# Performance work log

Hardware: AMD Instinct MI355X
Metric: run time of the kernel (lower is better)

## Reference

```python
import jax, jax.numpy as jnp
import numpy as np

B, GH, GW, DIM, NH = 1, 48, 64, 1536, 16
HD = DIM // NH          # 96
C = HD // 2             # 48, divisible by 3 as the rope split requires
L = max(GH, GW)


def setup_inputs() -> dict:
    key = jax.random.key(0)
    ks = jax.random.split(key, 6)
    x = jax.random.normal(ks[0], (B, GH * GW, DIM), jnp.float32)
    w_init = lambda k: jax.random.normal(k, (DIM, DIM), jnp.float32) * 0.02
    # rope frequency table: theta[p, j] = p / 10000^(j/C); freqs = exp(i*theta)
    pos = jnp.arange(L, dtype=jnp.float32)[:, None]
    inv = 10000.0 ** (-jnp.arange(C, dtype=jnp.float32) / C)
    theta = pos * inv[None, :]
    return {
        "x": x,
        "wq": w_init(ks[1]), "bq": jnp.zeros((DIM,), jnp.float32),
        "wk": w_init(ks[2]), "bk": jnp.zeros((DIM,), jnp.float32),
        "wv": w_init(ks[3]), "bv": jnp.zeros((DIM,), jnp.float32),
        "wo": w_init(ks[4]), "bo": jnp.zeros((DIM,), jnp.float32),
        "freqs_cos": jnp.cos(theta), "freqs_sin": jnp.sin(theta),
        "h": GH, "w": GW,
    }


def rope_apply_spatial(x, freqs_cos, freqs_sin, h, w):
    # x: [b, s, n, d] with s == h*w. Complex rotation done in real arithmetic.
    b, s, n, d = x.shape
    c = d // 2
    c3 = c // 3
    # channel groups: [0:c3] identity (ones), [c3:2c3] rotated by h-position,
    # [2c3:3c3] rotated by w-position  (matches freqs.split + cat in torch)
    cos_hw = jnp.concatenate([
        jnp.ones((h, w, c3), x.dtype),
        jnp.broadcast_to(freqs_cos[:h, None, c3:2 * c3], (h, w, c3)),
        jnp.broadcast_to(freqs_cos[None, :w, 2 * c3:3 * c3], (h, w, c3)),
    ], axis=-1).reshape(1, s, 1, c)
    sin_hw = jnp.concatenate([
        jnp.zeros((h, w, c3), x.dtype),
        jnp.broadcast_to(freqs_sin[:h, None, c3:2 * c3], (h, w, c3)),
        jnp.broadcast_to(freqs_sin[None, :w, 2 * c3:3 * c3], (h, w, c3)),
    ], axis=-1).reshape(1, s, 1, c)
    xc = x.reshape(b, s, n, c, 2)
    xr, xi = xc[..., 0], xc[..., 1]
    yr = xr * cos_hw - xi * sin_hw
    yi = xr * sin_hw + xi * cos_hw
    return jnp.stack([yr, yi], axis=-1).reshape(b, s, n, d)


def reference(x, wq, bq, wk, bk, wv, bv, wo, bo, freqs_cos, freqs_sin, h, w):
    b, s, _ = x.shape
    q = (x @ wq + bq).reshape(b, s, NH, HD)
    k = (x @ wk + bk).reshape(b, s, NH, HD)
    v = (x @ wv + bv).reshape(b, s, NH, HD)
    q = rope_apply_spatial(q, freqs_cos, freqs_sin, h, w)
    k = rope_apply_spatial(k, freqs_cos, freqs_sin, h, w)
    scale = 1.0 / jnp.sqrt(jnp.asarray(HD, q.dtype))
    scores = jnp.einsum('bqnd,bknd->bnqk', q, k) * scale  # [b, n, s, s]
    attn = jax.nn.softmax(scores, axis=-1)
    out = jnp.einsum('bnqk,bknd->bqnd', attn, v).reshape(b, s, NH * HD)
    return out @ wo + bo
```

## Files before the change

kernel.cpp:

```cpp
#include <hip/hip_runtime.h>
#include <math.h>

#define S_LEN 3072
#define DIM 1536
#define NHEADS 16
#define HDIM 96
#define NPAIR 48

typedef __attribute__((ext_vector_type(8))) _Float16 half8;
typedef __attribute__((ext_vector_type(4))) _Float16 half4v;
typedef __attribute__((ext_vector_type(2))) _Float16 half2v;
typedef __attribute__((ext_vector_type(4))) float f32x4;

__device__ inline void gload16(const void* g, void* l) {
    __builtin_amdgcn_global_load_lds(
        (const __attribute__((address_space(1))) void*)g,
        (__attribute__((address_space(3))) void*)l, 16, 0, 0);
}

__device__ inline uint4 gld128(const _Float16* p) {
    uint4 r;
    asm volatile("global_load_dwordx4 %0, %1, off"
                 : "=v"(r) : "v"(p));
    return r;
}

__global__ __launch_bounds__(256)
void convert_f32_f16(const float* __restrict__ src, _Float16* __restrict__ dst, int n4)
{
    int i = blockIdx.x * 256 + threadIdx.x;
    if (i < n4) {
        float4 v = *(const float4*)&src[(size_t)i * 4];
        half4v h = { (_Float16)v.x, (_Float16)v.y, (_Float16)v.z, (_Float16)v.w };
        *(half4v*)&dst[(size_t)i * 4] = h;
    }
}

__global__ __launch_bounds__(256)
void transpose_w(const float* __restrict__ w0, const float* __restrict__ w1,
                 const float* __restrict__ w2, const float* __restrict__ w3,
                 _Float16* __restrict__ wt)
{
    __shared__ _Float16 t[64][68];
    const int z = blockIdx.z;
    const float* W = (z == 0) ? w0 : (z == 1) ? w1 : (z == 2) ? w2 : w3;
    _Float16* O = wt + (size_t)z * DIM * DIM;
    const int k0 = blockIdx.y * 64, n0 = blockIdx.x * 64;
    const int tid = threadIdx.x;
    const int r = tid >> 4, c4 = (tid & 15) * 4;
#pragma unroll
    for (int g = 0; g < 4; g++) {
        int kk = r + g * 16;
        float4 v = *(const float4*)&W[(size_t)(k0 + kk) * DIM + n0 + c4];
        t[c4 + 0][kk] = (_Float16)v.x; t[c4 + 1][kk] = (_Float16)v.y;
        t[c4 + 2][kk] = (_Float16)v.z; t[c4 + 3][kk] = (_Float16)v.w;
    }
    __syncthreads();
    const int nr = tid >> 2, ks = (tid & 3) * 16;
#pragma unroll
    for (int s = 0; s < 4; s++)
        *(ushort4*)&O[(size_t)(n0 + nr) * DIM + k0 + ks + s * 4] =
            *(ushort4*)&t[nr][ks + s * 4];
}

template<bool QKV>
__global__ __launch_bounds__(512, 1)
void gemm256_f16(const _Float16* __restrict__ X,
                 const _Float16* __restrict__ W0t, const _Float16* __restrict__ W1t,
                 const _Float16* __restrict__ W2t,
                 const float* __restrict__ B0, const float* __restrict__ B1,
                 const float* __restrict__ B2,
                 const float* __restrict__ fc, const float* __restrict__ fs,
                 void* __restrict__ outv)
{
    __shared__ __align__(16) _Float16 AsB[2][256 * 64];
    __shared__ __align__(16) _Float16 BsB[2][256 * 64];

    const int tid = threadIdx.x;
    const int w = tid >> 6, lane = tid & 63;
    const int ln = lane & 15, quad = lane >> 4;
    const int bz = blockIdx.z;
    const _Float16* Wt = W0t; const float* bias = B0;
    if (QKV) { if (bz == 1) { Wt = W1t; bias = B1; } else if (bz == 2) { Wt = W2t; bias = B2; } }
    const int m0 = blockIdx.y * 256, n0 = blockIdx.x * 256;
    const int wm = w >> 2, wn = w & 3;
    const int row8 = lane >> 3, gch = (lane & 7) ^ row8;

    f32x4 acc[8][4];
#pragma unroll
    for (int i = 0; i < 8; i++)
#pragma unroll
        for (int j = 0; j < 4; j++) acc[i][j] = (f32x4){0.f, 0.f, 0.f, 0.f};

#pragma unroll
    for (int j = 0; j < 4; j++) {
        const int r = w * 32 + j * 8;
        gload16(X  + (size_t)(m0 + r + row8) * DIM + 0 + gch * 8, &AsB[0][r * 64]);
        gload16(Wt + (size_t)(n0 + r + row8) * DIM + 0 + gch * 8, &BsB[0][r * 64]);
    }
    asm volatile("s_waitcnt vmcnt(0)");
    __syncthreads();

    const int NKT = DIM / 64;
    for (int kt = 0; kt < NKT; ++kt) {
        const int cur = kt & 1;
        if (kt + 1 < NKT) {
            const int k0 = (kt + 1) * 64;
#pragma unroll
            for (int j = 0; j < 4; j++) {
                const int r = w * 32 + j * 8;
                gload16(X  + (size_t)(m0 + r + row8) * DIM + k0 + gch * 8, &AsB[cur ^ 1][r * 64]);
                gload16(Wt + (size_t)(n0 + r + row8) * DIM + k0 + gch * 8, &BsB[cur ^ 1][r * 64]);
            }
            __builtin_amdgcn_sched_barrier(0);
        }

#pragma unroll
        for (int ks = 0; ks < 2; ks++) {
            const int s8 = (((ks * 4 + quad) ^ (ln & 7))) * 8;
            half8 a[8], b[4];
#pragma unroll
            for (int mt = 0; mt < 8; mt++)
                a[mt] = *(const half8*)&AsB[cur][(wm * 128 + mt * 16 + ln) * 64 + s8];
#pragma unroll
            for (int nt = 0; nt < 4; nt++)
                b[nt] = *(const half8*)&BsB[cur][(wn * 64 + nt * 16 + ln) * 64 + s8];
#pragma unroll
            for (int mt = 0; mt < 8; mt++)
#pragma unroll
                for (int nt = 0; nt < 4; nt++)
                    acc[mt][nt] = __builtin_amdgcn_mfma_f32_16x16x32_f16(
                        a[mt], b[nt], acc[mt][nt], 0, 0, 0);
        }

        asm volatile("s_waitcnt vmcnt(0)");
        __syncthreads();
    }

#pragma unroll
    for (int nt = 0; nt < 4; nt++) {
        int col = n0 + wn * 64 + nt * 16 + ln;
        float bv = bias[col];
        int head = col / HDIM, hd = col % HDIM;
        int jc = hd >> 1;
        bool isreal = (ln & 1) == 0;
#pragma unroll
        for (int mt = 0; mt < 8; mt++) {
            int row0 = m0 + wm * 128 + mt * 16 + quad * 4;
            if (QKV && bz == 2) {
                half4v p;
#pragma unroll
                for (int r = 0; r < 4; r++) p[r] = (_Float16)(acc[mt][nt][r] + bv);
                *(half4v*)&((_Float16*)outv)[(((size_t)2 * NHEADS + head) * HDIM + hd) * S_LEN + row0] = p;
            } else if (QKV) {
                float v[4], vp[4];
#pragma unroll
                for (int r = 0; r < 4; r++) v[r] = acc[mt][nt][r] + bv;
#pragma unroll
                for (int r = 0; r < 4; r++) vp[r] = __shfl_xor(v[r], 1);
#pragma unroll
                for (int r = 0; r < 4; r++) {
                    int srow = row0 + r;
                    int pos = (jc < 32) ? (srow >> 6) : (srow & 63);
                    float c  = fc[pos * NPAIR + jc];
                    float sn = fs[pos * NPAIR + jc];
                    float xr = isreal ? v[r] : vp[r];
                    float xi = isreal ? vp[r] : v[r];
                    float rot = isreal ? (xr * c - xi * sn) : (xr * sn + xi * c);
                    float outval = (jc < 16) ? v[r] : rot;
                    ((_Float16*)outv)[(((size_t)bz * NHEADS + head) * S_LEN + srow) * HDIM + hd]
                        = (_Float16)outval;
                }
            } else {
#pragma unroll
                for (int r = 0; r < 4; r++)
                    ((float*)outv)[(size_t)(row0 + r) * DIM + col] = acc[mt][nt][r] + bv;
            }
        }
    }
}

__global__ __launch_bounds__(256, 2)
void attn_mfma_kernel(const _Float16* __restrict__ qh, const _Float16* __restrict__ kh,
                      const _Float16* __restrict__ vtg, _Float16* __restrict__ aoh)
{
    __shared__ __align__(16) _Float16 Kb[2][2][64 * 96];
    __shared__ __align__(16) _Float16 Vt[2][96][72];

    const int tid  = threadIdx.x;
    const int wid  = tid >> 6;
    const int p    = wid >> 1;
    const int wp   = wid & 1;
    const int lane = tid & 63;
    const int ln   = lane & 15;
    const int quad = lane >> 4;
    const int h    = blockIdx.y;
    const int q0   = blockIdx.x * 64;
    const float scale_ = 0.10206207261596577f * 1.4426950408889634f;
    const int NT = (S_LEN / 2) / 64;

    half8 aq[2][3];
#pragma unroll
    for (int qs = 0; qs < 2; qs++) {
        const _Float16* qrow = qh + (((size_t)h * S_LEN) + q0 + (wp * 2 + qs) * 16 + ln) * HDIM;
#pragma unroll
        for (int kb = 0; kb < 3; kb++) {
            half8 a = *(const half8*)&qrow[kb * 32 + quad * 8];
            half8 v;
#pragma unroll
            for (int i = 0; i < 8; i++) v[i] = (_Float16)((float)a[i] * scale_);
            aq[qs][kb] = v;
        }
    }

    f32x4 o[2][6];
#pragma unroll
    for (int qs = 0; qs < 2; qs++)
#pragma unroll
        for (int dn = 0; dn < 6; dn++) o[qs][dn] = (f32x4){0.f, 0.f, 0.f, 0.f};
    float m_[2] = {-INFINITY, -INFINITY}, l_[2] = {0.f, 0.f};

    const char* kbase = (const char*)(kh + ((size_t)h * S_LEN + p * (S_LEN / 2)) * HDIM);

    int koffb[6];
#pragma unroll
    for (int i = 0; i < 6; i++) {
        int pc = i * 128 + (tid & 127);
        int r  = pc / 12, c = pc - r * 12;
        int rm = r % 12;
        int cl = c - rm; if (cl < 0) cl += 12;
        koffb[i] = r * 192 + cl * 16;
    }
    const int A0 = (quad + ln) % 12;
    int ksel[3];
    ksel[0] = A0 * 16;
    { int t1 = A0 + 4; if (t1 >= 12) t1 -= 12; ksel[1] = t1 * 16; }
    { int t2 = A0 + 8; if (t2 >= 12) t2 -= 12; ksel[2] = t2 * 16; }

    const int tp = tid & 127;
    const int vd0 = tp >> 3, vc = tp & 7;
    const _Float16* vsrc0 = vtg + (size_t)h * HDIM * S_LEN + (size_t)vd0 * S_LEN
                          + p * (S_LEN / 2) + vc * 8;
    _Float16* vdst = &Vt[p][vd0][(vc ^ (vd0 & 7)) * 8];

#pragma unroll
    for (int i = 0; i < 6; i++)
        gload16(kbase + koffb[i], &Kb[p][0][i * 1024 + wp * 512]);
    uint4 vp0, vp1, vp2, vp3, vp4, vp5;
    vp0 = gld128(vsrc0 + 0 * 16 * S_LEN);
    vp1 = gld128(vsrc0 + 1 * 16 * S_LEN);
    vp2 = gld128(vsrc0 + 2 * 16 * S_LEN);
    vp3 = gld128(vsrc0 + 3 * 16 * S_LEN);
    vp4 = gld128(vsrc0 + 4 * 16 * S_LEN);
    vp5 = gld128(vsrc0 + 5 * 16 * S_LEN);
    asm volatile("s_waitcnt vmcnt(0)" ::: "memory");
    __builtin_amdgcn_sched_barrier(0);
    *(uint4*)(vdst + 0 * 16 * 72) = vp0;  *(uint4*)(vdst + 1 * 16 * 72) = vp1;
    *(uint4*)(vdst + 2 * 16 * 72) = vp2;  *(uint4*)(vdst + 3 * 16 * 72) = vp3;
    *(uint4*)(vdst + 4 * 16 * 72) = vp4;  *(uint4*)(vdst + 5 * 16 * 72) = vp5;
    __syncthreads();

    for (int kt = 0; kt < NT; ++kt) {
        const int cur = kt & 1;
        if (kt + 1 < NT) {
            const char* ks2 = kbase + (size_t)(kt + 1) * 12288;
#pragma unroll
            for (int i = 0; i < 6; i++)
                gload16(ks2 + koffb[i], &Kb[p][cur ^ 1][i * 1024 + wp * 512]);
            const _Float16* vs2 = vsrc0 + (kt + 1) * 64;
            vp0 = gld128(vs2 + 0 * 16 * S_LEN);
            vp1 = gld128(vs2 + 1 * 16 * S_LEN);
            vp2 = gld128(vs2 + 2 * 16 * S_LEN);
            vp3 = gld128(vs2 + 3 * 16 * S_LEN);
            vp4 = gld128(vs2 + 4 * 16 * S_LEN);
            vp5 = gld128(vs2 + 5 * 16 * S_LEN);
            __builtin_amdgcn_sched_barrier(0);
        }

        const char* Kc = (const char*)&Kb[p][cur][0];
        f32x4 s[2][4];
#pragma unroll
        for (int nb = 0; nb < 4; nb++) {
            const char* krow = Kc + (nb * 16 + ln) * 192;
            half8 ak0 = *(const half8*)(krow + ksel[(nb + 0) % 3]);
            half8 ak1 = *(const half8*)(krow + ksel[(nb + 1) % 3]);
            half8 ak2 = *(const half8*)(krow + ksel[(nb + 2) % 3]);
#pragma unroll
            for (int qs = 0; qs < 2; qs++) {
                f32x4 acc = (f32x4){0.f, 0.f, 0.f, 0.f};
                acc = __builtin_amdgcn_mfma_f32_16x16x32_f16(ak0, aq[qs][0], acc, 0, 0, 0);
                acc = __builtin_amdgcn_mfma_f32_16x16x32_f16(ak1, aq[qs][1], acc, 0, 0, 0);
                acc = __builtin_amdgcn_mfma_f32_16x16x32_f16(ak2, aq[qs][2], acc, 0, 0, 0);
                s[qs][nb] = acc;
            }
        }

        half4v ap[2][4];
#pragma unroll
        for (int qs = 0; qs < 2; qs++) {
            float ma = fmaxf(fmaxf(s[qs][0][0], s[qs][0][1]), fmaxf(s[qs][0][2], s[qs][0][3]));
            float mb = fmaxf(fmaxf(s[qs][1][0], s[qs][1][1]), fmaxf(s[qs][1][2], s[qs][1][3]));
            float mc = fmaxf(fmaxf(s[qs][2][0], s[qs][2][1]), fmaxf(s[qs][2][2], s[qs][2][3]));
            float md = fmaxf(fmaxf(s[qs][3][0], s[qs][3][1]), fmaxf(s[qs][3][2], s[qs][3][3]));
            float mx = fmaxf(fmaxf(ma, mb), fmaxf(mc, md));
            if (!__all(mx <= m_[qs] + 8.0f)) {
                mx = fmaxf(mx, __shfl_xor(mx, 16));
                mx = fmaxf(mx, __shfl_xor(mx, 32));
                float mn = fmaxf(m_[qs], mx);
                float al = __builtin_amdgcn_exp2f(m_[qs] - mn);
                m_[qs] = mn;
                l_[qs] *= al;
#pragma unroll
                for (int dn = 0; dn < 6; dn++)
#pragma unroll
                    for (int r = 0; r < 4; r++) o[qs][dn][r] *= al;
            }
            float rs = 0.f;
            float mq = m_[qs];
#pragma unroll
            for (int nb = 0; nb < 4; nb++) {
                float p0 = __builtin_amdgcn_exp2f(s[qs][nb][0] - mq);
                float p1 = __builtin_amdgcn_exp2f(s[qs][nb][1] - mq);
                float p2 = __builtin_amdgcn_exp2f(s[qs][nb][2] - mq);
                float p3 = __builtin_amdgcn_exp2f(s[qs][nb][3] - mq);
                rs += (p0 + p1) + (p2 + p3);
                half4v pk = { (_Float16)p0, (_Float16)p1, (_Float16)p2, (_Float16)p3 };
                ap[qs][nb] = pk;
            }
            l_[qs] += rs;
        }

#pragma unroll
        for (int nb = 0; nb < 4; nb++) {
            const int off = (((nb * 2 + (quad >> 1)) ^ (ln & 7)) * 8) + (quad & 1) * 4;
#pragma unroll
            for (int dn = 0; dn < 6; dn++) {
                half4v av = *(const half4v*)&Vt[p][dn * 16 + ln][off];
                o[0][dn] = __builtin_amdgcn_mfma_f32_16x16x16f16(av, ap[0][nb], o[0][dn], 0, 0, 0);
                o[1][dn] = __builtin_amdgcn_mfma_f32_16x16x16f16(av, ap[1][nb], o[1][dn], 0, 0, 0);
            }
        }

        __syncthreads();
        asm volatile("s_waitcnt vmcnt(0)" ::: "memory");
        __builtin_amdgcn_sched_barrier(0);
        if (kt + 1 < NT) {
            *(uint4*)(vdst + 0 * 16 * 72) = vp0;  *(uint4*)(vdst + 1 * 16 * 72) = vp1;
            *(uint4*)(vdst + 2 * 16 * 72) = vp2;  *(uint4*)(vdst + 3 * 16 * 72) = vp3;
            *(uint4*)(vdst + 4 * 16 * 72) = vp4;  *(uint4*)(vdst + 5 * 16 * 72) = vp5;
        }
        __syncthreads();
    }

    float lt[2];
#pragma unroll
    for (int qs = 0; qs < 2; qs++) {
        float l = l_[qs];
        l += __shfl_xor(l, 16);
        l += __shfl_xor(l, 32);
        lt[qs] = l;
    }
    float*  scr = (float*)&Kb[0][0][0];
    float2* mlb = (float2*)((char*)&Kb[0][0][0] + 26624);
    if (p == 1) {
#pragma unroll
        for (int qs = 0; qs < 2; qs++) {
            int row = (wp * 2 + qs) * 16 + ln;
            if (quad == 0) mlb[row] = make_float2(m_[qs], lt[qs]);
#pragma unroll
            for (int dn = 0; dn < 6; dn++)
                *(f32x4*)&scr[row * 100 + dn * 16 + quad * 4] = o[qs][dn];
        }
    }
    __syncthreads();
    if (p == 0) {
#pragma unroll
        for (int qs = 0; qs < 2; qs++) {
            int row = (wp * 2 + qs) * 16 + ln;
            float2 ml1 = mlb[row];
            float mm = fmaxf(m_[qs], ml1.x);
            float a0 = __builtin_amdgcn_exp2f(m_[qs] - mm);
            float a1 = __builtin_amdgcn_exp2f(ml1.x - mm);
            float li = 1.0f / (lt[qs] * a0 + ml1.y * a1);
            const size_t rowbase = (size_t)(q0 + row) * DIM + h * HDIM;
#pragma unroll
            for (int dn = 0; dn < 6; dn++) {
                f32x4 o1 = *(const f32x4*)&scr[row * 100 + dn * 16 + quad * 4];
                half4v pk;
#pragma unroll
                for (int r = 0; r < 4; r++)
                    pk[r] = (_Float16)((o[qs][dn][r] * a0 + o1[r] * a1) * li);
                *(half4v*)&aoh[rowbase + dn * 16 + quad * 4] = pk;
            }
        }
    }
}

extern "C" void kernel_launch(void* const* d_in, const int* in_sizes, int n_in,
                              void* d_out, int out_size, void* d_ws, size_t ws_size,
                              hipStream_t stream) {
    const float* x  = (const float*)d_in[0];
    const float* wq = (const float*)d_in[1];
    const float* bq = (const float*)d_in[2];
    const float* wk = (const float*)d_in[3];
    const float* bk = (const float*)d_in[4];
    const float* wv = (const float*)d_in[5];
    const float* bv = (const float*)d_in[6];
    const float* wo = (const float*)d_in[7];
    const float* bo = (const float*)d_in[8];
    const float* fc = (const float*)d_in[9];
    const float* fs = (const float*)d_in[10];
    float* out = (float*)d_out;

    const size_t per  = (size_t)NHEADS * S_LEN * HDIM;
    const size_t dim2 = (size_t)DIM * DIM;
    _Float16* hws  = (_Float16*)d_ws;
    _Float16* qkvh = hws;
    _Float16* qh   = qkvh;
    _Float16* kh   = qkvh + per;
    _Float16* vth  = qkvh + 2 * per;
    _Float16* xh   = hws + 3 * per;
    _Float16* wth  = hws + 4 * per;

    convert_f32_f16<<<(int)((S_LEN * DIM / 4 + 255) / 256), 256, 0, stream>>>(
        x, xh, S_LEN * DIM / 4);
    transpose_w<<<dim3(DIM / 64, DIM / 64, 4), 256, 0, stream>>>(wq, wk, wv, wo, wth);

    gemm256_f16<true><<<dim3(DIM / 256, S_LEN / 256, 3), 512, 0, stream>>>(
        xh, wth, wth + dim2, wth + 2 * dim2, bq, bk, bv, fc, fs, qkvh);
    attn_mfma_kernel<<<dim3(S_LEN / 64, NHEADS), 256, 0, stream>>>(qh, kh, vth, xh);
    gemm256_f16<false><<<dim3(DIM / 256, S_LEN / 256, 1), 512, 0, stream>>>(
        xh, wth + 3 * dim2, nullptr, nullptr, bo, nullptr, nullptr, fc, fs, out);
}
```

Measured before the change: 335.5 us.

## Deepen GEMM prefetch with partial vmcnt waits, XCD-aware block remap, smaller out-proj tile

Restructures the GEMM main loop so the load for tile kt+2 is issued right after the compute barrier, and waits use partial vmcnt counts instead of draining all outstanding loads. This keeps one tile's global-to-LDS transfer in flight during compute. The 1D grid is remapped so consecutive blocks on the same XCD get neighbouring tiles, improving L2 reuse. The output projection uses 128-row tiles, giving 144 workgroups instead of 72 to fill more CUs. The cost is a more fragile hand-tuned wait count and less per-block reuse in the output GEMM.

```diff
diff --git a/kernel.cpp b/kernel.cpp
--- a/kernel.cpp
+++ b/kernel.cpp
@@ -63,80 +63,96 @@
             *(ushort4*)&t[nr][ks + s * 4];
 }
 
-template<bool QKV>
+template<bool QKV, int BM>
 __global__ __launch_bounds__(512, 1)
-void gemm256_f16(const _Float16* __restrict__ X,
-                 const _Float16* __restrict__ W0t, const _Float16* __restrict__ W1t,
-                 const _Float16* __restrict__ W2t,
-                 const float* __restrict__ B0, const float* __restrict__ B1,
-                 const float* __restrict__ B2,
-                 const float* __restrict__ fc, const float* __restrict__ fs,
-                 void* __restrict__ outv)
+void gemm_pipe_f16(const _Float16* __restrict__ X,
+                   const _Float16* __restrict__ W0t, const _Float16* __restrict__ W1t,
+                   const _Float16* __restrict__ W2t,
+                   const float* __restrict__ B0, const float* __restrict__ B1,
+                   const float* __restrict__ B2,
+                   const float* __restrict__ fc, const float* __restrict__ fs,
+                   void* __restrict__ outv)
 {
-    __shared__ __align__(16) _Float16 AsB[2][256 * 64];
-    __shared__ __align__(16) _Float16 BsB[2][256 * 64];
+    constexpr int MT = BM / 32;
+    constexpr int AJ = BM / 64;
+    __shared__ __align__(16) _Float16 As[2][BM * 64];
+    __shared__ __align__(16) _Float16 Bs[2][256 * 64];
 
     const int tid = threadIdx.x;
     const int w = tid >> 6, lane = tid & 63;
     const int ln = lane & 15, quad = lane >> 4;
-    const int bz = blockIdx.z;
+    const int row8 = lane >> 3, gch = (lane & 7) ^ row8;
+
+    const int nwg = gridDim.x;
+    const int wk = (blockIdx.x & 7) * (nwg >> 3) + (blockIdx.x >> 3);
+    int m0, n0, bz;
+    if (QKV) {
+        const int m = wk % 12, nz = wk / 12;
+        m0 = m * 256; n0 = (nz % 6) * 256; bz = nz / 6;
+    } else {
+        m0 = (wk % 24) * 128; n0 = (wk / 24) * 256; bz = 0;
+    }
     const _Float16* Wt = W0t; const float* bias = B0;
     if (QKV) { if (bz == 1) { Wt = W1t; bias = B1; } else if (bz == 2) { Wt = W2t; bias = B2; } }
-    const int m0 = blockIdx.y * 256, n0 = blockIdx.x * 256;
-    const int wm = w >> 2, wn = w & 3;
-    const int row8 = lane >> 3, gch = (lane & 7) ^ row8;
-
-    f32x4 acc[8][4];
-#pragma unroll
-    for (int i = 0; i < 8; i++)
+
+    f32x4 acc[MT][4];
+#pragma unroll
+    for (int i = 0; i < MT; i++)
 #pragma unroll
         for (int j = 0; j < 4; j++) acc[i][j] = (f32x4){0.f, 0.f, 0.f, 0.f};
 
-#pragma unroll
-    for (int j = 0; j < 4; j++) {
-        const int r = w * 32 + j * 8;
-        gload16(X  + (size_t)(m0 + r + row8) * DIM + 0 + gch * 8, &AsB[0][r * 64]);
-        gload16(Wt + (size_t)(n0 + r + row8) * DIM + 0 + gch * 8, &BsB[0][r * 64]);
-    }
-    asm volatile("s_waitcnt vmcnt(0)");
-    __syncthreads();
+    auto stage = [&](int k0, int d) {
+#pragma unroll
+        for (int j = 0; j < AJ; j++) {
+            const int r = w * (BM / 8) + j * 8;
+            gload16(X + (size_t)(m0 + r + row8) * DIM + k0 + gch * 8, &As[d][r * 64]);
+        }
+#pragma unroll
+        for (int j = 0; j < 4; j++) {
+            const int r = w * 32 + j * 8;
+            gload16(Wt + (size_t)(n0 + r + row8) * DIM + k0 + gch * 8, &Bs[d][r * 64]);
+        }
+        __builtin_amdgcn_sched_barrier(0);
+    };
+
+    stage(0, 0);
+    stage(64, 1);
 
     const int NKT = DIM / 64;
     for (int kt = 0; kt < NKT; ++kt) {
         const int cur = kt & 1;
-        if (kt + 1 < NKT) {
-            const int k0 = (kt + 1) * 64;
-#pragma unroll
-            for (int j = 0; j < 4; j++) {
-                const int r = w * 32 + j * 8;
-                gload16(X  + (size_t)(m0 + r + row8) * DIM + k0 + gch * 8, &AsB[cur ^ 1][r * 64]);
-                gload16(Wt + (size_t)(n0 + r + row8) * DIM + k0 + gch * 8, &BsB[cur ^ 1][r * 64]);
-            }
-            __builtin_amdgcn_sched_barrier(0);
-        }
+        if (kt == NKT - 1)       asm volatile("s_waitcnt vmcnt(0)" ::: "memory");
+        else if constexpr (BM == 256) asm volatile("s_waitcnt vmcnt(8)" ::: "memory");
+        else                     asm volatile("s_waitcnt vmcnt(6)" ::: "memory");
+        __builtin_amdgcn_sched_barrier(0);
+        __builtin_amdgcn_s_barrier();
+        __builtin_amdgcn_sched_barrier(0);
 
 #pragma unroll
         for (int ks = 0; ks < 2; ks++) {
             const int s8 = (((ks * 4 + quad) ^ (ln & 7))) * 8;
-            half8 a[8], b[4];
-#pragma unroll
-            for (int mt = 0; mt < 8; mt++)
-                a[mt] = *(const half8*)&AsB[cur][(wm * 128 + mt * 16 + ln) * 64 + s8];
+            half8 a[MT], b[4];
+#pragma unroll
+            for (int mt = 0; mt < MT; mt++)
+                a[mt] = *(const half8*)&As[cur][((w >> 2) * (BM / 2) + mt * 16 + ln) * 64 + s8];
 #pragma unroll
             for (int nt = 0; nt < 4; nt++)
-                b[nt] = *(const half8*)&BsB[cur][(wn * 64 + nt * 16 + ln) * 64 + s8];
-#pragma unroll
-            for (int mt = 0; mt < 8; mt++)
+                b[nt] = *(const half8*)&Bs[cur][((w & 3) * 64 + nt * 16 + ln) * 64 + s8];
+#pragma unroll
+            for (int mt = 0; mt < MT; mt++)
 #pragma unroll
                 for (int nt = 0; nt < 4; nt++)
                     acc[mt][nt] = __builtin_amdgcn_mfma_f32_16x16x32_f16(
                         a[mt], b[nt], acc[mt][nt], 0, 0, 0);
         }
 
-        asm volatile("s_waitcnt vmcnt(0)");
-        __syncthreads();
-    }
-
+        __builtin_amdgcn_sched_barrier(0);
+        __builtin_amdgcn_s_barrier();
+        __builtin_amdgcn_sched_barrier(0);
+        if (kt + 2 < NKT) stage((kt + 2) * 64, cur);
+    }
+
+    const int wm = w >> 2, wn = w & 3;
 #pragma unroll
     for (int nt = 0; nt < 4; nt++) {
         int col = n0 + wn * 64 + nt * 16 + ln;
@@ -145,8 +161,8 @@
         int jc = hd >> 1;
         bool isreal = (ln & 1) == 0;
 #pragma unroll
-        for (int mt = 0; mt < 8; mt++) {
-            int row0 = m0 + wm * 128 + mt * 16 + quad * 4;
+        for (int mt = 0; mt < MT; mt++) {
+            int row0 = m0 + wm * (BM / 2) + mt * 16 + quad * 4;
             if (QKV && bz == 2) {
                 half4v p;
 #pragma unroll
@@ -426,9 +442,9 @@
         x, xh, S_LEN * DIM / 4);
     transpose_w<<<dim3(DIM / 64, DIM / 64, 4), 256, 0, stream>>>(wq, wk, wv, wo, wth);
 
-    gemm256_f16<true><<<dim3(DIM / 256, S_LEN / 256, 3), 512, 0, stream>>>(
+    gemm_pipe_f16<true, 256><<<216, 512, 0, stream>>>(
         xh, wth, wth + dim2, wth + 2 * dim2, bq, bk, bv, fc, fs, qkvh);
     attn_mfma_kernel<<<dim3(S_LEN / 64, NHEADS), 256, 0, stream>>>(qh, kh, vth, xh);
-    gemm256_f16<false><<<dim3(DIM / 256, S_LEN / 256, 1), 512, 0, stream>>>(
+    gemm_pipe_f16<false, 128><<<144, 512, 0, stream>>>(
         xh, wth + 3 * dim2, nullptr, nullptr, bo, nullptr, nullptr, fc, fs, out);
 }
```

Result: faster. 323.7 us (-3.5%).
